# Performance work log

Hardware: AMD Instinct MI355X
Metric: run time of the kernel (lower is better)

## Reference

```python
import jax, jax.numpy as jnp
import numpy as np

B, H, W, C = 64, 56, 56, 192
NH, WS, SS = 6, 7, 3          # heads, window size, shift size
N = WS * WS                   # tokens per window = 49
NW = (H // WS) * (W // WS)    # windows per image = 64
HD = C // NH                  # head dim = 32
SCALE = HD ** -0.5
EPS = 1e-5


def _rel_pos_index():
    coords = np.stack(np.meshgrid(np.arange(WS), np.arange(WS), indexing='ij'))  # [2,WS,WS]
    flat = coords.reshape(2, -1)                                                  # [2,N]
    rel = (flat[:, :, None] - flat[:, None, :]).transpose(1, 2, 0)                # [N,N,2]
    rel[..., 0] += WS - 1
    rel[..., 1] += WS - 1
    rel[..., 0] *= 2 * WS - 1
    return jnp.asarray(rel.sum(-1))  # [N,N] int

REL_IDX = _rel_pos_index()


def _shift_mask():
    # standard Swin shifted-window attention mask: 0 within region, -100 across
    img = np.zeros((H, W), dtype=np.float32)
    cnt = 0
    for hs in (slice(0, -WS), slice(-WS, -SS), slice(-SS, None)):
        for ws in (slice(0, -WS), slice(-WS, -SS), slice(-SS, None)):
            img[hs, ws] = cnt
            cnt += 1
    win = img.reshape(H // WS, WS, W // WS, WS).transpose(0, 2, 1, 3).reshape(NW, N)
    diff = win[:, None, :] - win[:, :, None]
    return jnp.asarray(np.where(diff != 0, -100.0, 0.0).astype(np.float32))  # [NW,N,N]


def setup_inputs() -> dict:
    key = jax.random.key(0)
    ks = jax.random.split(key, 8)
    s = 0.02
    return {
        'x': jax.random.normal(ks[0], (B, H, W, C), jnp.float32),
        'mask_matrix': _shift_mask(),
        'norm1_g': jnp.ones((C,), jnp.float32),
        'norm1_b': jnp.zeros((C,), jnp.float32),
        'qkv_w': jax.random.normal(ks[1], (3 * C, C), jnp.float32) * s,
        'qkv_b': jnp.zeros((3 * C,), jnp.float32),
        'rpb_table': jax.random.normal(ks[2], ((2 * WS - 1) ** 2, NH), jnp.float32) * s,
        'proj_w': jax.random.normal(ks[3], (C, C), jnp.float32) * s,
        'proj_b': jnp.zeros((C,), jnp.float32),
        'norm2_g': jnp.ones((C,), jnp.float32),
        'norm2_b': jnp.zeros((C,), jnp.float32),
        'fc1_w': jax.random.normal(ks[4], (4 * C, C), jnp.float32) * s,
        'fc1_b': jnp.zeros((4 * C,), jnp.float32),
        'fc2_w': jax.random.normal(ks[5], (C, 4 * C), jnp.float32) * s,
        'fc2_b': jnp.zeros((C,), jnp.float32),
    }


def _ln(x, g, b):
    m = jnp.mean(x, axis=-1, keepdims=True)
    v = jnp.mean(jnp.square(x - m), axis=-1, keepdims=True)
    return (x - m) * jax.lax.rsqrt(v + EPS) * g + b


def _block(x, mask_matrix, norm1_g, norm1_b, qkv_w, qkv_b, rpb_table,
           proj_w, proj_b, norm2_g, norm2_b, fc1_w, fc1_b, fc2_w, fc2_b):
    shortcut = x
    xn = _ln(x, norm1_g, norm1_b)
    # cyclic shift
    xs = jnp.roll(xn, (-SS, -SS), axis=(1, 2))
    # window partition -> [B*NW, N, C]
    win = xs.reshape(B, H // WS, WS, W // WS, WS, C).transpose(0, 1, 3, 2, 4, 5).reshape(B * NW, N, C)
    # qkv projection
    qkv = jnp.einsum('wnc,dc->wnd', win, qkv_w) + qkv_b           # [B*NW, N, 3C]
    qkv = qkv.reshape(B * NW, N, 3, NH, HD).transpose(2, 0, 3, 1, 4)
    q, k, v = qkv[0], qkv[1], qkv[2]                               # [B*NW, NH, N, HD]
    attn = jnp.einsum('whqd,whkd->whqk', q * SCALE, k)             # [B*NW, NH, N, N]
    # relative position bias gather
    bias = rpb_table[REL_IDX.reshape(-1)].reshape(N, N, NH).transpose(2, 0, 1)  # [NH,N,N]
    attn = attn + bias[None]
    # shifted-window mask
    attn = attn.reshape(B, NW, NH, N, N) + mask_matrix[None, :, None]
    attn = jax.nn.softmax(attn.reshape(B * NW, NH, N, N), axis=-1)
    out = jnp.einsum('whqk,whkd->whqd', attn, v)                   # [B*NW, NH, N, HD]
    out = out.transpose(0, 2, 1, 3).reshape(B * NW, N, C)
    out = jnp.einsum('wnc,dc->wnd', out, proj_w) + proj_b
    # window reverse + reverse shift
    xr = out.reshape(B, H // WS, W // WS, WS, WS, C).transpose(0, 1, 3, 2, 4, 5).reshape(B, H, W, C)
    xr = jnp.roll(xr, (SS, SS), axis=(1, 2))
    x = shortcut + xr
    # MLP
    xn2 = _ln(x, norm2_g, norm2_b)
    h = jax.nn.gelu(jnp.einsum('bhwc,dc->bhwd', xn2, fc1_w) + fc1_b, approximate=False)
    x = x + jnp.einsum('bhwd,cd->bhwc', h, fc2_w) + fc2_b
    return x


def reference(x, mask_matrix, norm1_g, norm1_b, qkv_w, qkv_b, rpb_table,
              proj_w, proj_b, norm2_g, norm2_b, fc1_w, fc1_b, fc2_w, fc2_b):
    return _block(x, mask_matrix, norm1_g, norm1_b, qkv_w, qkv_b, rpb_table,
                  proj_w, proj_b, norm2_g, norm2_b, fc1_w, fc1_b, fc2_w, fc2_b)
```

## Files before the change

kernel.cpp:

```cpp
#include <hip/hip_runtime.h>
#include <hip/hip_bf16.h>
#include <math.h>

typedef __attribute__((ext_vector_type(8))) short s16x8;
typedef __attribute__((ext_vector_type(4))) float f32x4;

static constexpr float cSCALE = 0.17677669529663687f;

__device__ __forceinline__ float bf2f(unsigned short u) {
    union { unsigned int i; float f; } c; c.i = ((unsigned int)u) << 16; return c.f;
}
__device__ __forceinline__ unsigned short f2bf(float f) {
    union { float f; unsigned int i; } c; c.f = f;
    unsigned int r = c.i + (0x7fffu + ((c.i >> 16) & 1u));
    return (unsigned short)(r >> 16);
}
__device__ __forceinline__ unsigned pk2(float a, float b) {
    unsigned r;
    asm("v_cvt_pk_bf16_f32 %0, %1, %2" : "=v"(r) : "v"(a), "v"(b));
    return r;
}
__device__ __forceinline__ s16x8 cvt8(const float4 a, const float4 b) {
    s16x8 r;
    r[0]=(short)f2bf(a.x); r[1]=(short)f2bf(a.y); r[2]=(short)f2bf(a.z); r[3]=(short)f2bf(a.w);
    r[4]=(short)f2bf(b.x); r[5]=(short)f2bf(b.y); r[6]=(short)f2bf(b.z); r[7]=(short)f2bf(b.w);
    return r;
}
__device__ __forceinline__ float gelu_f(float t) {
    const float u = 1.5957691216057308f * t * (1.0f + 0.044715f * t * t);
    return t / (1.0f + __expf(-u));
}

#define GLDS16(gp, lp) __builtin_amdgcn_global_load_lds( \
    (const __attribute__((address_space(1))) void*)(gp), \
    (__attribute__((address_space(3))) void*)(lp), 16, 0, 0)

__device__ __forceinline__ void ln_frag(const float* __restrict__ rowp,
                                        const float* __restrict__ g,
                                        const float* __restrict__ b,
                                        int hi, s16x8* xa)
{
    float4 v[12];
    #pragma unroll
    for (int k = 0; k < 6; ++k) {
        v[2*k]   = *(const float4*)(rowp + k*32 + hi*8);
        v[2*k+1] = *(const float4*)(rowp + k*32 + hi*8 + 4);
    }
    float sm = 0.f, sq = 0.f;
    #pragma unroll
    for (int i = 0; i < 12; ++i) {
        sm += (v[i].x + v[i].y) + (v[i].z + v[i].w);
        sq += (v[i].x*v[i].x + v[i].y*v[i].y) + (v[i].z*v[i].z + v[i].w*v[i].w);
    }
    sm += __shfl_xor(sm, 16); sq += __shfl_xor(sq, 16);
    sm += __shfl_xor(sm, 32); sq += __shfl_xor(sq, 32);
    const float mean = sm * (1.0f/192.0f);
    const float rstd = rsqrtf(sq * (1.0f/192.0f) - mean*mean + 1e-5f);
    #pragma unroll
    for (int k = 0; k < 6; ++k) {
        const float4 ga = *(const float4*)(g + k*32 + hi*8);
        const float4 gb = *(const float4*)(g + k*32 + hi*8 + 4);
        const float4 ba = *(const float4*)(b + k*32 + hi*8);
        const float4 bb = *(const float4*)(b + k*32 + hi*8 + 4);
        union { s16x8 s; unsigned u[4]; } r;
        r.u[0] = pk2((v[2*k].x  -mean)*rstd*ga.x + ba.x, (v[2*k].y  -mean)*rstd*ga.y + ba.y);
        r.u[1] = pk2((v[2*k].z  -mean)*rstd*ga.z + ba.z, (v[2*k].w  -mean)*rstd*ga.w + ba.w);
        r.u[2] = pk2((v[2*k+1].x-mean)*rstd*gb.x + bb.x, (v[2*k+1].y-mean)*rstd*gb.y + bb.y);
        r.u[3] = pk2((v[2*k+1].z-mean)*rstd*gb.z + bb.z, (v[2*k+1].w-mean)*rstd*gb.w + bb.w);
        xa[k] = r.s;
    }
}

__global__ __launch_bounds__(256)
void pack_w(const float* __restrict__ qkvw, const float* __restrict__ pw,
            const float* __restrict__ f1w, const float* __restrict__ f2w,
            unsigned short* __restrict__ o)
{
    const int t = blockIdx.x * 256 + threadIdx.x;
    const int lane = t & 63, f = t >> 6;
    const int ln = lane & 15, ko = (lane >> 4) * 8;
    const float* src;
    if (f < 216) {
        const int h = f / 36, r = f - h * 36, nf = r / 6, kf = r - nf * 6;
        src = qkvw + (size_t)((nf >> 1) * 192 + h * 32 + (nf & 1) * 16 + ln) * 192 + kf * 32 + ko;
    } else if (f < 288) {
        const int g = f - 216, h = g / 12, nf = g - h * 12;
        src = pw + (size_t)(nf * 16 + ln) * 192 + h * 32 + ko;
    } else {
        const int g = f - 288;
        const int c = g / 24, r24 = g - c * 24;
        if (r24 < 12) {
            const int nf = r24 / 6, kf = r24 - nf * 6;
            src = f1w + (size_t)(c * 32 + nf * 16 + ln) * 192 + kf * 32 + ko;
        } else {
            const int nf = r24 - 12;
            src = f2w + (size_t)(nf * 16 + ln) * 768 + c * 32 + ko;
        }
    }
    *(s16x8*)(o + (size_t)t * 8) = cvt8(*(const float4*)src, *(const float4*)(src + 4));
}

__global__ __launch_bounds__(256)
void pack_bias(const float* __restrict__ mask, const float* __restrict__ rpb,
               unsigned short* __restrict__ o)
{
    const int wi = blockIdx.x / 6, h = blockIdx.x - wi * 6;
    for (int t = threadIdx.x; t < 49 * 64; t += 256) {
        const int n = t >> 6, mm = t & 63;
        const int ln = mm >> 2, nf = mm & 3;
        const int m = nf * 16 + ln;
        float v = 0.f;
        if (m < 49) {
            const int p1 = n / 7, q1 = n - p1 * 7, p2 = m / 7, q2 = m - p2 * 7;
            const int ridx = (p1 - p2 + 6) * 13 + (q1 - q2 + 6);
            v = rpb[ridx * 6 + h] + mask[(size_t)wi * 2401 + n * 49 + m];
        }
        o[(size_t)(wi * 6 + h) * 49 * 64 + t] = f2bf(v);
    }
}

__global__ __launch_bounds__(256, 4)
void swin_attn(const float* __restrict__ x, const float* __restrict__ g1,
               const float* __restrict__ b1, const unsigned short* __restrict__ wp,
               const unsigned short* __restrict__ bias_g,
               const float* __restrict__ qkvb, const float* __restrict__ pb,
               float* __restrict__ y)
{
    __shared__ __align__(16) unsigned short q_[64][40];
    __shared__ __align__(16) unsigned short o_[64][40];
    __shared__ __align__(16) unsigned short k2_[2][64][40];
    __shared__ __align__(16) unsigned short vt2_[2][32][72];
    __shared__ __align__(16) unsigned short p_[64][72];

    const s16x8* wv = (const s16x8*)wp;
    const int w  = blockIdx.x;
    const int bb = w >> 6, wi = w & 63;
    const int wh = wi >> 3, ww = wi & 7;
    const int tid = threadIdx.x, lane = tid & 63, wave = tid >> 6;
    const int ln = lane & 15, hi = lane >> 4, ko = hi * 8, ro = hi * 4;
    const int m0 = wave * 16;

    s16x8 xa[6];
    {
        const int t = m0 + ln;
        const int p = t / 7, q7 = t - p * 7;
        int i2 = wh * 7 + p + 3;  if (i2 >= 56) i2 -= 56;
        int j2 = ww * 7 + q7 + 3; if (j2 >= 56) j2 -= 56;
        const float* xr = x + ((size_t)(bb * 56 + i2) * 56 + j2) * 192;
        ln_frag(xr, g1, b1, hi, xa);
        if (t >= 49) {
            #pragma unroll
            for (int k = 0; k < 6; ++k) xa[k] = s16x8{0,0,0,0,0,0,0,0};
        }
    }

    auto qkv_head = [&](int hh) {
        const s16x8* wq = wv + ((size_t)(hh * 36) << 6);
        #pragma unroll
        for (int nf = 0; nf < 6; ++nf) {
            s16x8 bf6[6];
            #pragma unroll
            for (int kf = 0; kf < 6; ++kf) bf6[kf] = wq[(nf * 6 + kf) * 64 + lane];
            f32x4 a = f32x4{0.f,0.f,0.f,0.f};
            #pragma unroll
            for (int kf = 0; kf < 6; ++kf)
                a = __builtin_amdgcn_mfma_f32_16x16x32_bf16(xa[kf], bf6[kf], a, 0, 0, 0);
            const int col = nf * 16 + ln;
            if (nf < 2) {
                const float bq = qkvb[hh*32 + col];
                const unsigned lo = pk2((a[0]+bq)*cSCALE, (a[1]+bq)*cSCALE);
                const unsigned hh2 = pk2((a[2]+bq)*cSCALE, (a[3]+bq)*cSCALE);
                q_[m0+ro+0][col] = (unsigned short)lo;  q_[m0+ro+1][col] = (unsigned short)(lo >> 16);
                q_[m0+ro+2][col] = (unsigned short)hh2; q_[m0+ro+3][col] = (unsigned short)(hh2 >> 16);
            } else if (nf < 4) {
                const float bk = qkvb[192 + hh*32 + col - 32];
                const unsigned lo = pk2(a[0]+bk, a[1]+bk), hh2 = pk2(a[2]+bk, a[3]+bk);
                k2_[hh&1][m0+ro+0][col-32] = (unsigned short)lo;  k2_[hh&1][m0+ro+1][col-32] = (unsigned short)(lo >> 16);
                k2_[hh&1][m0+ro+2][col-32] = (unsigned short)hh2; k2_[hh&1][m0+ro+3][col-32] = (unsigned short)(hh2 >> 16);
            } else {
                const float bv = qkvb[384 + hh*32 + col - 64];
                const unsigned lo = pk2(a[0]+bv, a[1]+bv), hh2 = pk2(a[2]+bv, a[3]+bv);
                vt2_[hh&1][col-64][m0+ro+0] = (unsigned short)lo;  vt2_[hh&1][col-64][m0+ro+1] = (unsigned short)(lo >> 16);
                vt2_[hh&1][col-64][m0+ro+2] = (unsigned short)hh2; vt2_[hh&1][col-64][m0+ro+3] = (unsigned short)(hh2 >> 16);
            }
        }
    };

    qkv_head(0);

    f32x4 accp[12];
    #pragma unroll
    for (int i = 0; i < 12; ++i) accp[i] = f32x4{0.f,0.f,0.f,0.f};

    uint2 bb4[4];
    {
        const unsigned short* bg = bias_g + (size_t)(wi * 6) * 3136;
        #pragma unroll
        for (int i = 0; i < 4; ++i) {
            const int nc = min(m0 + ro + i, 48);
            bb4[i] = *(const uint2*)(bg + nc * 64 + ln * 4);
        }
    }

    for (int h = 0; h < 6; ++h) {
        __syncthreads();

        f32x4 s4[4];
        {
            const s16x8 aq = *(const s16x8*)&q_[m0 + ln][ko];
            #pragma unroll
            for (int nf = 0; nf < 4; ++nf) {
                const s16x8 bk = *(const s16x8*)&k2_[h & 1][nf * 16 + ln][ko];
                s4[nf] = __builtin_amdgcn_mfma_f32_16x16x32_bf16(aq, bk, f32x4{0.f,0.f,0.f,0.f}, 0, 0, 0);
            }
        }
        float inv4[4];
        #pragma unroll
        for (int i = 0; i < 4; ++i) {
            const int n = m0 + ro + i;
            const uint2 u = bb4[i];
            float vv[4];
            vv[0] = (ln      >= 49) ? -1e30f : (s4[0][i] + bf2f((unsigned short)(u.x)));
            vv[1] = (16 + ln >= 49) ? -1e30f : (s4[1][i] + bf2f((unsigned short)(u.x >> 16)));
            vv[2] = (32 + ln >= 49) ? -1e30f : (s4[2][i] + bf2f((unsigned short)(u.y)));
            vv[3] = (48 + ln >= 49) ? -1e30f : (s4[3][i] + bf2f((unsigned short)(u.y >> 16)));
            const float e0 = __expf(vv[0]), e1 = __expf(vv[1]);
            const float e2 = __expf(vv[2]), e3 = __expf(vv[3]);
            float ssum = (e0 + e1) + (e2 + e3);
            #pragma unroll
            for (int o = 1; o < 16; o <<= 1) ssum += __shfl_xor(ssum, o);
            inv4[i] = 1.0f / ssum;
            const unsigned plo = pk2(e0, e1), phi = pk2(e2, e3);
            p_[n][     ln] = (unsigned short)plo;
            p_[n][16 + ln] = (unsigned short)(plo >> 16);
            p_[n][32 + ln] = (unsigned short)phi;
            p_[n][48 + ln] = (unsigned short)(phi >> 16);
        }

        {
            const int hn = (h < 5) ? h + 1 : 5;
            const unsigned short* bg = bias_g + (size_t)(wi * 6 + hn) * 3136;
            #pragma unroll
            for (int i = 0; i < 4; ++i) {
                const int nc = min(m0 + ro + i, 48);
                bb4[i] = *(const uint2*)(bg + nc * 64 + ln * 4);
            }
        }

        f32x4 o2[2];
        o2[0] = f32x4{0.f,0.f,0.f,0.f}; o2[1] = f32x4{0.f,0.f,0.f,0.f};
        #pragma unroll
        for (int kf = 0; kf < 2; ++kf) {
            const s16x8 ap = *(const s16x8*)&p_[m0 + ln][kf * 32 + ko];
            #pragma unroll
            for (int nf = 0; nf < 2; ++nf) {
                const s16x8 bv = *(const s16x8*)&vt2_[h & 1][nf * 16 + ln][kf * 32 + ko];
                o2[nf] = __builtin_amdgcn_mfma_f32_16x16x32_bf16(ap, bv, o2[nf], 0, 0, 0);
            }
        }
        #pragma unroll
        for (int nf = 0; nf < 2; ++nf) {
            const int col = nf * 16 + ln;
            const unsigned lo = pk2(o2[nf][0] * inv4[0], o2[nf][1] * inv4[1]);
            const unsigned hh2 = pk2(o2[nf][2] * inv4[2], o2[nf][3] * inv4[3]);
            o_[m0+ro+0][col] = (unsigned short)lo;  o_[m0+ro+1][col] = (unsigned short)(lo >> 16);
            o_[m0+ro+2][col] = (unsigned short)hh2; o_[m0+ro+3][col] = (unsigned short)(hh2 >> 16);
        }

        if (h < 5) qkv_head(h + 1);

        {
            const s16x8 ao = *(const s16x8*)&o_[m0 + ln][ko];
            const s16x8* wpj = wv + ((size_t)(216 + h * 12) << 6);
            #pragma unroll
            for (int half = 0; half < 2; ++half) {
                s16x8 bf6[6];
                #pragma unroll
                for (int nf = 0; nf < 6; ++nf) bf6[nf] = wpj[(half * 6 + nf) * 64 + lane];
                #pragma unroll
                for (int nf = 0; nf < 6; ++nf)
                    accp[half * 6 + nf] = __builtin_amdgcn_mfma_f32_16x16x32_bf16(
                        ao, bf6[nf], accp[half * 6 + nf], 0, 0, 0);
            }
        }
    }

    #pragma unroll
    for (int i = 0; i < 4; ++i) {
        const int n = m0 + ro + i;
        if (n < 49) {
            const int p = n / 7, q7 = n - p * 7;
            int i2 = wh * 7 + p + 3;  if (i2 >= 56) i2 -= 56;
            int j2 = ww * 7 + q7 + 3; if (j2 >= 56) j2 -= 56;
            const size_t base = ((size_t)(bb * 56 + i2) * 56 + j2) * 192;
            #pragma unroll
            for (int nf = 0; nf < 12; ++nf) {
                const int col = nf * 16 + ln;
                y[base + col] = x[base + col] + pb[col] + accp[nf][i];
            }
        }
    }
}

__device__ __forceinline__ void stage_fc1(const unsigned short* __restrict__ wp, int c,
                                          unsigned short* dst, int tid) {
    if (tid < 384) {
        const unsigned short* g = wp + (((size_t)(288 + c * 24)) << 9) + tid * 8;
        unsigned short* l = dst + tid * 8;
        GLDS16(g, l);
        GLDS16(g + 3072, l + 3072);
    }
}

__global__ __launch_bounds__(512, 4)
void swin_mlp(const float* __restrict__ g2, const float* __restrict__ b2,
              const unsigned short* __restrict__ wp,
              const float* __restrict__ f1b, const float* __restrict__ f2b,
              float* __restrict__ y)
{
    __shared__ __align__(16) unsigned short wbuf[2][6144];
    __shared__ __align__(16) unsigned short hb[128][40];
    __shared__ float f1b_l[768];
    __shared__ float f2b_l[192];

    const s16x8* wv = (const s16x8*)wp;
    const int tid = threadIdx.x, lane = tid & 63, wave = tid >> 6;
    const int ln = lane & 15, hi = lane >> 4, ko = hi * 8, ro = hi * 4;
    const int m0 = wave * 16;
    const size_t r0 = (size_t)blockIdx.x * 128;

    for (int t = tid; t < 768; t += 512) f1b_l[t] = f1b[t];
    for (int t = tid; t < 192; t += 512) f2b_l[t] = f2b[t];

    s16x8 xa[6];
    ln_frag(y + (r0 + m0 + ln) * 192, g2, b2, hi, xa);

    stage_fc1(wp, 0, wbuf[0], tid);
    stage_fc1(wp, 1, wbuf[1], tid);
    asm volatile("s_waitcnt lgkmcnt(0)" ::: "memory");

    f32x4 acc2[12];
    #pragma unroll
    for (int i = 0; i < 12; ++i) acc2[i] = f32x4{0.f,0.f,0.f,0.f};

    for (int c = 0; c < 24; ++c) {
        asm volatile("s_waitcnt vmcnt(2)" ::: "memory");
        __builtin_amdgcn_s_barrier();

        const s16x8* wb1 = (const s16x8*)wbuf[c & 1];
        f32x4 acc1[2];
        acc1[0] = f32x4{0.f,0.f,0.f,0.f}; acc1[1] = f32x4{0.f,0.f,0.f,0.f};
        #pragma unroll
        for (int kf = 0; kf < 6; ++kf) {
            #pragma unroll
            for (int nf = 0; nf < 2; ++nf)
                acc1[nf] = __builtin_amdgcn_mfma_f32_16x16x32_bf16(
                    xa[kf], wb1[(nf * 6 + kf) * 64 + lane], acc1[nf], 0, 0, 0);
        }
        #pragma unroll
        for (int nf = 0; nf < 2; ++nf) {
            const int col = nf * 16 + ln;
            const float bias = f1b_l[c * 32 + col];
            const unsigned lo = pk2(gelu_f(acc1[nf][0] + bias), gelu_f(acc1[nf][1] + bias));
            const unsigned hh2 = pk2(gelu_f(acc1[nf][2] + bias), gelu_f(acc1[nf][3] + bias));
            hb[m0+ro+0][col] = (unsigned short)lo;  hb[m0+ro+1][col] = (unsigned short)(lo >> 16);
            hb[m0+ro+2][col] = (unsigned short)hh2; hb[m0+ro+3][col] = (unsigned short)(hh2 >> 16);
        }
        const s16x8 ah = *(const s16x8*)&hb[m0 + ln][ko];
        const s16x8* wv2 = wv + ((size_t)(288 + c * 24 + 12) << 6);
        #pragma unroll
        for (int half = 0; half < 2; ++half) {
            s16x8 bf6[6];
            #pragma unroll
            for (int nf = 0; nf < 6; ++nf) bf6[nf] = wv2[(half * 6 + nf) * 64 + lane];
            #pragma unroll
            for (int nf = 0; nf < 6; ++nf)
                acc2[half * 6 + nf] = __builtin_amdgcn_mfma_f32_16x16x32_bf16(
                    ah, bf6[nf], acc2[half * 6 + nf], 0, 0, 0);
        }

        __builtin_amdgcn_s_barrier();
        if (c < 22) stage_fc1(wp, c + 2, wbuf[c & 1], tid);
    }

    #pragma unroll
    for (int i = 0; i < 4; ++i) {
        const int row = m0 + ro + i;
        float* yp = y + (r0 + row) * 192;
        #pragma unroll
        for (int nf = 0; nf < 12; ++nf) {
            const int col = nf * 16 + ln;
            yp[col] = yp[col] + f2b_l[col] + acc2[nf][i];
        }
    }
}

extern "C" void kernel_launch(void* const* d_in, const int* in_sizes, int n_in,
                              void* d_out, int out_size, void* d_ws, size_t ws_size,
                              hipStream_t stream) {
    (void)in_sizes; (void)n_in; (void)ws_size; (void)out_size;
    const float* x    = (const float*)d_in[0];
    const float* mask = (const float*)d_in[1];
    const float* g1   = (const float*)d_in[2];
    const float* b1   = (const float*)d_in[3];
    const float* qkvw = (const float*)d_in[4];
    const float* qkvb = (const float*)d_in[5];
    const float* rpb  = (const float*)d_in[6];
    const float* pw   = (const float*)d_in[7];
    const float* pb   = (const float*)d_in[8];
    const float* g2   = (const float*)d_in[9];
    const float* b2   = (const float*)d_in[10];
    const float* f1w  = (const float*)d_in[11];
    const float* f1b  = (const float*)d_in[12];
    const float* f2w  = (const float*)d_in[13];
    const float* f2b  = (const float*)d_in[14];
    float* y = (float*)d_out;
    unsigned short* wpk  = (unsigned short*)d_ws;
    unsigned short* bias = wpk + 442368;

    pack_w<<<dim3(216), dim3(256), 0, stream>>>(qkvw, pw, f1w, f2w, wpk);
    pack_bias<<<dim3(384), dim3(256), 0, stream>>>(mask, rpb, bias);
    swin_attn<<<dim3(64 * 64), dim3(256), 0, stream>>>(
        x, g1, b1, wpk, bias, qkvb, pb, y);
    swin_mlp<<<dim3(1568), dim3(512), 0, stream>>>(
        g2, b2, wpk, f1b, f2b, y);
}
```

Before: 571.8 us.

## Stage fc2 weights through LDS alongside fc1 and drop softmax padding selects

The MLP kernel now double-buffers both the fc1 and fc2 weight slices for each chunk into LDS using direct global-to-LDS loads, instead of reading the fc2 fragments from global memory inside the loop. This doubles the LDS weight buffer, which may lower occupancy, and adjusts the vmcnt waits and barriers to match. Separately, the padded bias columns are filled with -100 so the attention softmax can drop its per-element padding selects, relying on exp(-100) being negligible.

```diff
diff --git a/kernel.cpp b/kernel.cpp
--- a/kernel.cpp
+++ b/kernel.cpp
@@ -109,13 +109,13 @@
         const int n = t >> 6, mm = t & 63;
         const int ln = mm >> 2, nf = mm & 3;
         const int m = nf * 16 + ln;
-        float v = 0.f;
+        float v = -100.0f;
         if (m < 49) {
             const int p1 = n / 7, q1 = n - p1 * 7, p2 = m / 7, q2 = m - p2 * 7;
             const int ridx = (p1 - p2 + 6) * 13 + (q1 - q2 + 6);
             v = rpb[ridx * 6 + h] + mask[(size_t)wi * 2401 + n * 49 + m];
         }
-        o[(size_t)(wi * 6 + h) * 49 * 64 + t] = f2bf(v);
+        o[(size_t)(wi * 6 + h) * 3136 + t] = f2bf(v);
     }
 }
 
@@ -219,13 +219,10 @@
         for (int i = 0; i < 4; ++i) {
             const int n = m0 + ro + i;
             const uint2 u = bb4[i];
-            float vv[4];
-            vv[0] = (ln      >= 49) ? -1e30f : (s4[0][i] + bf2f((unsigned short)(u.x)));
-            vv[1] = (16 + ln >= 49) ? -1e30f : (s4[1][i] + bf2f((unsigned short)(u.x >> 16)));
-            vv[2] = (32 + ln >= 49) ? -1e30f : (s4[2][i] + bf2f((unsigned short)(u.y)));
-            vv[3] = (48 + ln >= 49) ? -1e30f : (s4[3][i] + bf2f((unsigned short)(u.y >> 16)));
-            const float e0 = __expf(vv[0]), e1 = __expf(vv[1]);
-            const float e2 = __expf(vv[2]), e3 = __expf(vv[3]);
+            const float e0 = __expf(s4[0][i] + bf2f((unsigned short)(u.x)));
+            const float e1 = __expf(s4[1][i] + bf2f((unsigned short)(u.x >> 16)));
+            const float e2 = __expf(s4[2][i] + bf2f((unsigned short)(u.y)));
+            const float e3 = __expf(s4[3][i] + bf2f((unsigned short)(u.y >> 16)));
             float ssum = (e0 + e1) + (e2 + e3);
             #pragma unroll
             for (int o = 1; o < 16; o <<= 1) ssum += __shfl_xor(ssum, o);
@@ -302,14 +299,13 @@
     }
 }
 
-__device__ __forceinline__ void stage_fc1(const unsigned short* __restrict__ wp, int c,
-                                          unsigned short* dst, int tid) {
-    if (tid < 384) {
-        const unsigned short* g = wp + (((size_t)(288 + c * 24)) << 9) + tid * 8;
-        unsigned short* l = dst + tid * 8;
-        GLDS16(g, l);
-        GLDS16(g + 3072, l + 3072);
-    }
+__device__ __forceinline__ void stage24k(const unsigned short* __restrict__ wp, int c,
+                                         unsigned short* dst, int tid) {
+    const unsigned short* g = wp + (((size_t)(288 + c * 24)) << 9) + tid * 8;
+    unsigned short* l = dst + tid * 8;
+    #pragma unroll
+    for (int i = 0; i < 3; ++i)
+        GLDS16(g + i * 4096, l + i * 4096);
 }
 
 __global__ __launch_bounds__(512, 4)
@@ -318,12 +314,11 @@
               const float* __restrict__ f1b, const float* __restrict__ f2b,
               float* __restrict__ y)
 {
-    __shared__ __align__(16) unsigned short wbuf[2][6144];
+    __shared__ __align__(16) unsigned short wbuf[2][12288];
     __shared__ __align__(16) unsigned short hb[128][40];
     __shared__ float f1b_l[768];
     __shared__ float f2b_l[192];
 
-    const s16x8* wv = (const s16x8*)wp;
     const int tid = threadIdx.x, lane = tid & 63, wave = tid >> 6;
     const int ln = lane & 15, hi = lane >> 4, ko = hi * 8, ro = hi * 4;
     const int m0 = wave * 16;
@@ -335,8 +330,8 @@
     s16x8 xa[6];
     ln_frag(y + (r0 + m0 + ln) * 192, g2, b2, hi, xa);
 
-    stage_fc1(wp, 0, wbuf[0], tid);
-    stage_fc1(wp, 1, wbuf[1], tid);
+    stage24k(wp, 0, wbuf[0], tid);
+    stage24k(wp, 1, wbuf[1], tid);
     asm volatile("s_waitcnt lgkmcnt(0)" ::: "memory");
 
     f32x4 acc2[12];
@@ -344,10 +339,11 @@
     for (int i = 0; i < 12; ++i) acc2[i] = f32x4{0.f,0.f,0.f,0.f};
 
     for (int c = 0; c < 24; ++c) {
-        asm volatile("s_waitcnt vmcnt(2)" ::: "memory");
+        if (c == 23) asm volatile("s_waitcnt vmcnt(0)" ::: "memory");
+        else         asm volatile("s_waitcnt vmcnt(3)" ::: "memory");
         __builtin_amdgcn_s_barrier();
 
-        const s16x8* wb1 = (const s16x8*)wbuf[c & 1];
+        const s16x8* wb = (const s16x8*)wbuf[c & 1];
         f32x4 acc1[2];
         acc1[0] = f32x4{0.f,0.f,0.f,0.f}; acc1[1] = f32x4{0.f,0.f,0.f,0.f};
         #pragma unroll
@@ -355,7 +351,7 @@
             #pragma unroll
             for (int nf = 0; nf < 2; ++nf)
                 acc1[nf] = __builtin_amdgcn_mfma_f32_16x16x32_bf16(
-                    xa[kf], wb1[(nf * 6 + kf) * 64 + lane], acc1[nf], 0, 0, 0);
+                    xa[kf], wb[(nf * 6 + kf) * 64 + lane], acc1[nf], 0, 0, 0);
         }
         #pragma unroll
         for (int nf = 0; nf < 2; ++nf) {
@@ -367,20 +363,15 @@
             hb[m0+ro+2][col] = (unsigned short)hh2; hb[m0+ro+3][col] = (unsigned short)(hh2 >> 16);
         }
         const s16x8 ah = *(const s16x8*)&hb[m0 + ln][ko];
-        const s16x8* wv2 = wv + ((size_t)(288 + c * 24 + 12) << 6);
-        #pragma unroll
-        for (int half = 0; half < 2; ++half) {
-            s16x8 bf6[6];
-            #pragma unroll
-            for (int nf = 0; nf < 6; ++nf) bf6[nf] = wv2[(half * 6 + nf) * 64 + lane];
-            #pragma unroll
-            for (int nf = 0; nf < 6; ++nf)
-                acc2[half * 6 + nf] = __builtin_amdgcn_mfma_f32_16x16x32_bf16(
-                    ah, bf6[nf], acc2[half * 6 + nf], 0, 0, 0);
-        }
-
-        __builtin_amdgcn_s_barrier();
-        if (c < 22) stage_fc1(wp, c + 2, wbuf[c & 1], tid);
+        #pragma unroll
+        for (int nf = 0; nf < 12; ++nf)
+            acc2[nf] = __builtin_amdgcn_mfma_f32_16x16x32_bf16(
+                ah, wb[(12 + nf) * 64 + lane], acc2[nf], 0, 0, 0);
+
+        if (c < 23) {
+            __builtin_amdgcn_s_barrier();
+            if (c < 22) stage24k(wp, c + 2, wbuf[c & 1], tid);
+        }
     }
 
     #pragma unroll
```

New measurement: 530.7 us. -7.2%, faster.
